# Performance work log

Measured on AMD Instinct MI355X. Metric: run time of the kernel, lower is better.

## Reference

```python
import jax, jax.numpy as jnp
import numpy as np

N_NODES = 50000
N_EDGES = 800000
IN_CH = 128
HID = 48
HEADS = 2
HH = HID * HEADS  # 96
N_GRAPHS = 64
NEG_SLOPE = 0.2


def _gat_layer(x, src, dst, n, W, a_src, a_dst, b, heads, out_ch):
    # x: [N, in]; W: [in, heads*out]; a_src/a_dst: [heads, out]; b: [heads*out]
    h = (x @ W).reshape(n, heads, out_ch)              # [N, H, C]
    es = (h * a_src).sum(-1)                            # [N, H]
    ed = (h * a_dst).sum(-1)                            # [N, H]
    e = jax.nn.leaky_relu(es[src] + ed[dst], NEG_SLOPE)  # [E, H]
    m = jax.ops.segment_max(e, dst, num_segments=n)      # segment softmax (stable)
    p = jnp.exp(e - m[dst])
    denom = jax.ops.segment_sum(p, dst, num_segments=n)
    alpha = p / denom[dst]                               # [E, H]
    out = jax.ops.segment_sum(alpha[:, :, None] * h[src], dst, num_segments=n)
    return out.reshape(n, heads * out_ch) + b


def setup_inputs() -> dict:
    key = jax.random.key(0)
    ks = jax.random.split(key, 20)
    x = jax.random.normal(ks[0], (N_NODES, IN_CH), dtype=jnp.float32)
    edge_index = jax.random.randint(ks[1], (2, N_EDGES), 0, N_NODES, dtype=jnp.int64)
    edge_weight = jax.random.uniform(ks[2], (N_EDGES,), dtype=jnp.float32)
    batch = jnp.sort(jax.random.randint(ks[3], (N_NODES,), 0, N_GRAPHS, dtype=jnp.int64))
    s = 0.1
    params = {
        'W1': jax.random.normal(ks[4], (IN_CH, HH)) * s,
        'as1': jax.random.normal(ks[5], (HEADS, HID)) * s,
        'ad1': jax.random.normal(ks[6], (HEADS, HID)) * s,
        'b1': jnp.zeros((HH,), jnp.float32),
        'W2': jax.random.normal(ks[7], (HH, HH)) * s,
        'as2': jax.random.normal(ks[8], (1, HH)) * s,
        'ad2': jax.random.normal(ks[9], (1, HH)) * s,
        'b2': jnp.zeros((HH,), jnp.float32),
        'W3': jax.random.normal(ks[10], (HH, HH)) * s,
        'as3': jax.random.normal(ks[11], (1, HH)) * s,
        'ad3': jax.random.normal(ks[12], (1, HH)) * s,
        'b3': jnp.zeros((HH,), jnp.float32),
        'W4': jax.random.normal(ks[13], (HH, HH)) * s,
        'as4': jax.random.normal(ks[14], (1, HH)) * s,
        'ad4': jax.random.normal(ks[15], (1, HH)) * s,
        'b4': jnp.zeros((HH,), jnp.float32),
        'Wc': jax.random.normal(ks[16], (HH, 1)) * s,
        'bc': jnp.zeros((1,), jnp.float32),
    }
    return {'x': x, 'edge_index': edge_index, 'edge_weight': edge_weight,
            'batch': batch, **params}


def reference(x, edge_index, edge_weight, batch,
              W1, as1, ad1, b1, W2, as2, ad2, b2,
              W3, as3, ad3, b3, W4, as4, ad4, b4, Wc, bc):
    n = x.shape[0]
    loops = jnp.arange(n, dtype=edge_index.dtype)  # PyG GATConv add_self_loops=True
    src = jnp.concatenate([edge_index[0], loops])
    dst = jnp.concatenate([edge_index[1], loops])
    # edge_weight is ignored by GATConv when edge_dim=None (faithful to PyG)
    h = jax.nn.relu(_gat_layer(x, src, dst, n, W1, as1, ad1, b1, HEADS, HID))
    h = jax.nn.relu(_gat_layer(h, src, dst, n, W2, as2, ad2, b2, 1, HH))
    h = jax.nn.relu(_gat_layer(h, src, dst, n, W3, as3, ad3, b3, 1, HH))
    h = jax.nn.relu(_gat_layer(h, src, dst, n, W4, as4, ad4, b4, 1, HH))
    # global_mean_pool
    sums = jax.ops.segment_sum(h, batch, num_segments=N_GRAPHS)
    cnts = jax.ops.segment_sum(jnp.ones((n, 1), h.dtype), batch, num_segments=N_GRAPHS)
    pooled = sums / jnp.maximum(cnts, 1.0)
    return jax.nn.sigmoid(pooled @ Wc + bc)
```

## Files before the change

### kernel.cpp

```cpp
#include <hip/hip_runtime.h>
#include <hip/hip_bf16.h>

#define NN 50000
#define NE 800000
#define NG 64
#define NBUCK 256
#define BN 196
#define EPB 4096
#define HB 196
#define SMAX 4200

typedef __attribute__((ext_vector_type(8))) short short8;
typedef __attribute__((ext_vector_type(4))) float float4v;
typedef __attribute__((ext_vector_type(2))) float float2v;

__device__ __forceinline__ float bf2f(unsigned short u){
    unsigned v = ((unsigned)u) << 16; float f; __builtin_memcpy(&f, &v, 4); return f;
}
__device__ __forceinline__ unsigned short f2bf(float f){
    unsigned u; __builtin_memcpy(&u, &f, 4);
    u = (u + 0x7fffu + ((u >> 16) & 1u)) >> 16;
    return (unsigned short)u;
}
__device__ __forceinline__ float lrelu(float v){ return v > 0.f ? v : 0.2f * v; }

__device__ __forceinline__ float ldflex(const void* p, long i, int isbf){
    if (isbf) return bf2f(((const unsigned short*)p)[i]);
    return ((const float*)p)[i];
}
__device__ __forceinline__ int ldidx(const int* p, long i, int is64){
    return p[is64 ? (i << 1) : i];
}

__device__ __forceinline__ unsigned int enc_fp8_1(float f){
    unsigned u; __builtin_memcpy(&u, &f, 4);
    unsigned s = (u >> 24) & 0x80u;
    float a = fabsf(f); a = fminf(a, 448.f);
    float x = a * 0x1p-120f;
    unsigned xu; __builtin_memcpy(&xu, &x, 4);
    unsigned r = (xu + 0x7FFFFu + ((xu >> 20) & 1u)) >> 20;
    if (r > 0x7Eu) r = 0x7Eu;
    return s | r;
}
__device__ __forceinline__ unsigned short pk_fp8(float a, float b){
#if __has_builtin(__builtin_amdgcn_cvt_pk_fp8_f32)
    int r = __builtin_amdgcn_cvt_pk_fp8_f32(a, b, 0, false);
    return (unsigned short)(r & 0xFFFF);
#else
    return (unsigned short)(enc_fp8_1(a) | (enc_fp8_1(b) << 8));
#endif
}
__device__ __forceinline__ float dec_fp8_manual(unsigned int byte){
    unsigned bits = ((byte & 0x80u) << 24) | ((byte & 0x7Fu) << 20);
    float f; __builtin_memcpy(&f, &bits, 4);
    return f * 0x1p120f;
}
__device__ __forceinline__ void dec_fp8x4_pk(unsigned int v, float2v& lo, float2v& hi){
#if __has_builtin(__builtin_amdgcn_cvt_pk_f32_fp8)
    lo = __builtin_amdgcn_cvt_pk_f32_fp8((int)v, false);
    hi = __builtin_amdgcn_cvt_pk_f32_fp8((int)v, true);
#else
    lo[0] = dec_fp8_manual(v & 0xFF);
    lo[1] = dec_fp8_manual((v >> 8) & 0xFF);
    hi[0] = dec_fp8_manual((v >> 16) & 0xFF);
    hi[1] = dec_fp8_manual((v >> 24) & 0xFF);
#endif
}

__device__ __forceinline__ float rdlane_f(float v, int l){
    int i; __builtin_memcpy(&i, &v, 4);
    int r = __builtin_amdgcn_readlane(i, l);
    float f; __builtin_memcpy(&f, &r, 4);
    return f;
}

__global__ void detect_kernel(const unsigned short* xu, const unsigned int* eiu,
                              const unsigned int* bu, int* flags, int* bcnt,
                              float* pooled, int* gcnt){
    if (blockIdx.x == 1){
        int tid = threadIdx.x;
        bcnt[tid] = 0;
        for (int i = tid; i < NG * 96; i += 256) pooled[i] = 0.f;
        if (tid < NG) gcnt[tid] = 0;
        return;
    }
    if (threadIdx.x != 0) return;
    int hit = 0;
    for (int i = 0; i < 128; i++){
        int ex = (xu[2 * i] >> 7) & 0xFF;
        if (ex >= 100 && ex <= 140) hit++;
    }
    flags[0] = (hit >= 64) ? 1 : 0;
    int z = 0;
    for (int i = 0; i < 128; i++) if (eiu[2 * i + 1] == 0) z++;
    flags[1] = (z >= 120) ? 1 : 0;
    z = 0;
    for (int i = 0; i < 128; i++) if (bu[49745 + 2 * i] == 0) z++;
    flags[2] = (z >= 120) ? 1 : 0;
}

__global__ __launch_bounds__(256) void wtprep_kernel(const void* W0, const void* W1,
                                                     const void* W2, const void* W3,
                                                     unsigned short* wt_all,
                                                     const int* flags){
    int l = blockIdx.x;
    const void* W = (l == 0) ? W0 : (l == 1) ? W1 : (l == 2) ? W2 : W3;
    int K = (l == 0) ? 128 : 96;
    unsigned short* out = wt_all + ((l == 0) ? 0 : (96 * 128 + (l - 1) * 96 * 96));
    int isbf = flags[0];
    int tot = 96 * K;
    for (int i = threadIdx.x; i < tot; i += 256){
        int c = i / K, k = i - c * K;
        out[i] = f2bf(ldflex(W, (long)k * 96 + c, isbf));
    }
}

__global__ __launch_bounds__(256) void bhist_kernel(const int* __restrict__ ei,
                                                    int* __restrict__ bcnt,
                                                    const int* __restrict__ flags){
    __shared__ int h[NBUCK];
    int tid = threadIdx.x;
    h[tid] = 0; __syncthreads();
    int f64 = flags[1];
    long e0 = (long)blockIdx.x * EPB + tid;
    #pragma unroll
    for (int r = 0; r < 16; r++){
        long e = e0 + r * 256;
        if (e < NE){
            int d = ldidx(ei, NE + e, f64);
            atomicAdd(&h[d / BN], 1);
        }
    }
    __syncthreads();
    atomicAdd(&bcnt[tid], h[tid]);
}

__global__ __launch_bounds__(256) void bscan_kernel(const int* __restrict__ bcnt,
                                                    int* __restrict__ bbase,
                                                    int* __restrict__ bcur){
    __shared__ int sd[NBUCK];
    int tid = threadIdx.x;
    int v = bcnt[tid];
    sd[tid] = v; __syncthreads();
    for (int off = 1; off < 256; off <<= 1){
        int x = sd[tid];
        int y = (tid >= off) ? sd[tid - off] : 0;
        __syncthreads();
        sd[tid] = x + y;
        __syncthreads();
    }
    int excl = sd[tid] - v;
    bbase[tid] = excl;
    bcur[tid] = excl;
    if (tid == 255) bbase[256] = excl + v;
}

__global__ __launch_bounds__(256) void bscatter_kernel(const int* __restrict__ ei,
                                                       int* __restrict__ bcur,
                                                       int2* __restrict__ ebuf,
                                                       const int* __restrict__ flags){
    __shared__ int h[NBUCK], lofs[NBUCK], gbase[NBUCK], lcur[NBUCK];
    __shared__ int2 lstage[EPB];
    int tid = threadIdx.x;
    int f64 = flags[1];
    h[tid] = 0; __syncthreads();
    int2 ed[16]; int bk[16];
    long e0 = (long)blockIdx.x * EPB + tid;
    #pragma unroll
    for (int r = 0; r < 16; r++){
        long e = e0 + r * 256;
        if (e < NE){
            int s = ldidx(ei, e, f64);
            int d = ldidx(ei, NE + e, f64);
            ed[r] = make_int2(s, d);
            bk[r] = d / BN;
            atomicAdd(&h[bk[r]], 1);
        } else bk[r] = -1;
    }
    __syncthreads();
    int v = h[tid];
    lofs[tid] = v; __syncthreads();
    for (int off = 1; off < 256; off <<= 1){
        int x = lofs[tid];
        int y = (tid >= off) ? lofs[tid - off] : 0;
        __syncthreads();
        lofs[tid] = x + y;
        __syncthreads();
    }
    int excl = lofs[tid] - v;
    lofs[tid] = excl;
    lcur[tid] = excl;
    if (v > 0) gbase[tid] = atomicAdd(&bcur[tid], v);
    __syncthreads();
    #pragma unroll
    for (int r = 0; r < 16; r++){
        if (bk[r] >= 0){
            int p = atomicAdd(&lcur[bk[r]], 1);
            lstage[p] = ed[r];
        }
    }
    __syncthreads();
    long base = (long)blockIdx.x * EPB;
    int cnt = (NE - base < EPB) ? (int)(NE - base) : EPB;
    for (int j = tid; j < cnt; j += 256){
        int2 e = lstage[j];
        int i = e.y / BN;
        ebuf[gbase[i] + j - lofs[i]] = e;
    }
}

__global__ __launch_bounds__(256) void place_kernel(const int2* __restrict__ ebuf,
                                                    const int* __restrict__ bbase,
                                                    int* __restrict__ row_ptr,
                                                    int2* __restrict__ csr2){
    __shared__ int nh[BN];
    __shared__ int nofs[256];
    __shared__ int lcur[BN];
    __shared__ int2 stage[SMAX];
    int k = blockIdx.x, tid = threadIdx.x;
    int n0 = k * BN;
    int seg0 = bbase[k], len = bbase[k + 1] - seg0;
    for (int i = tid; i < BN; i += 256) nh[i] = 0;
    __syncthreads();
    for (int j = tid; j < len; j += 256){
        int2 e = ebuf[seg0 + j];
        atomicAdd(&nh[e.y - n0], 1);
    }
    __syncthreads();
    int v = (tid < BN) ? nh[tid] : 0;
    nofs[tid] = v; __syncthreads();
    for (int off = 1; off < 256; off <<= 1){
        int x = nofs[tid];
        int y = (tid >= off) ? nofs[tid - off] : 0;
        __syncthreads();
        nofs[tid] = x + y;
        __syncthreads();
    }
    int excl = nofs[tid] - v;
    if (tid < BN){
        lcur[tid] = excl;
        int node = n0 + tid;
        if (node < NN) row_ptr[node] = seg0 + excl;
    }
    if (k == NBUCK - 1 && tid == 0) row_ptr[NN] = NE;
    __syncthreads();
    if (len <= SMAX){
        for (int j = tid; j < len; j += 256){
            int2 e = ebuf[seg0 + j];
            int p = atomicAdd(&lcur[e.y - n0], 1);
            stage[p] = e;
        }
        __syncthreads();
        for (int j = tid; j < len; j += 256)
            csr2[seg0 + j] = stage[j];
    } else {
        for (int j = tid; j < len; j += 256){
            int2 e = ebuf[seg0 + j];
            int p = atomicAdd(&lcur[e.y - n0], 1);
            csr2[seg0 + p] = e;
        }
    }
}

template<int K, int H, bool L1>
__global__ __launch_bounds__(256) void gemm_mfma(const void* __restrict__ Ain,
                                                 const unsigned short* __restrict__ Wt,
                                                 const void* __restrict__ as_,
                                                 const void* __restrict__ ad_,
                                                 unsigned short* __restrict__ hq16,
                                                 float* __restrict__ es,
                                                 float* __restrict__ ed,
                                                 float* __restrict__ pself,
                                                 const int* __restrict__ flags){
    __shared__ union {
        struct { unsigned short xs[64 * 40]; unsigned short wt[96 * 40]; } s;
        float hs[64 * 104];
    } u;
    int tid = threadIdx.x;
    int row0 = blockIdx.x * 64;
    int lane = tid & 63, w = tid >> 6;
    int m = lane & 15, q = lane >> 4;
    int isbf = flags[0];
    float4v acc[6];
    #pragma unroll
    for (int ct = 0; ct < 6; ct++) acc[ct] = (float4v){0.f, 0.f, 0.f, 0.f};

    int sr = tid >> 2, kp = tid & 3;
    int rr = row0 + sr; if (rr >= NN) rr = NN - 1;

    for (int k0 = 0; k0 < K; k0 += 32){
        uint4 av;
        if (L1 && !isbf){
            const float* xf = (const float*)Ain + (size_t)rr * K + k0 + kp * 8;
            float4 f1 = *(const float4*)xf;
            float4 f2 = *(const float4*)(xf + 4);
            av.x = (unsigned)f2bf(f1.x) | ((unsigned)f2bf(f1.y) << 16);
            av.y = (unsigned)f2bf(f1.z) | ((unsigned)f2bf(f1.w) << 16);
            av.z = (unsigned)f2bf(f2.x) | ((unsigned)f2bf(f2.y) << 16);
            av.w = (unsigned)f2bf(f2.z) | ((unsigned)f2bf(f2.w) << 16);
        } else {
            av = *(const uint4*)((const unsigned short*)Ain + (size_t)rr * K + k0 + kp * 8);
        }
        *(uint4*)(u.s.xs + sr * 40 + kp * 8) = av;
        for (int i = tid; i < 96 * 4; i += 256){
            int c = i >> 2, kq = i & 3;
            *(uint4*)(u.s.wt + c * 40 + kq * 8) =
                *(const uint4*)(Wt + (size_t)c * K + k0 + kq * 8);
        }
        __syncthreads();
        short8 a = *(const short8*)(u.s.xs + (w * 16 + m) * 40 + q * 8);
        #pragma unroll
        for (int ct = 0; ct < 6; ct++){
            short8 b = *(const short8*)(u.s.wt + (ct * 16 + m) * 40 + q * 8);
            acc[ct] = __builtin_amdgcn_mfma_f32_16x16x32_bf16(a, b, acc[ct], 0, 0, 0);
        }
        __syncthreads();
    }

    #pragma unroll
    for (int ct = 0; ct < 6; ct++)
        #pragma unroll
        for (int r = 0; r < 4; r++)
            u.hs[(w * 16 + q * 4 + r) * 104 + ct * 16 + m] = acc[ct][r];
    __syncthreads();

    int rl = tid >> 2, part = tid & 3;
    int row = row0 + rl;
    float hv[24];
    #pragma unroll
    for (int jj = 0; jj < 6; jj++)
        *(float4v*)&hv[jj * 4] = *(const float4v*)&u.hs[rl * 104 + part * 24 + jj * 4];

    float pes = 0.f, ped = 0.f;
    #pragma unroll
    for (int i = 0; i < 24; i++){
        int c = part * 24 + i;
        pes += hv[i] * ldflex(as_, c, isbf);
        ped += hv[i] * ldflex(ad_, c, isbf);
    }
    pes += __shfl_xor(pes, 1); ped += __shfl_xor(ped, 1);
    if (H == 1){ pes += __shfl_xor(pes, 2); ped += __shfl_xor(ped, 2); }

    if (row < NN){
        if (part == 0){
            es[(long)row * H] = pes; ed[(long)row * H] = ped;
            pself[(long)row * H] = __expf(lrelu(pes + ped));
        }
        if (H == 2 && part == 2){
            es[(long)row * H + 1] = pes; ed[(long)row * H + 1] = ped;
            pself[(long)row * H + 1] = __expf(lrelu(pes + ped));
        }
        unsigned short wds[12];
        #pragma unroll
        for (int j = 0; j < 12; j++) wds[j] = pk_fp8(hv[2 * j], hv[2 * j + 1]);
        uint2* dst = (uint2*)hq16 + (long)row * 16 + part * 3;
        #pragma unroll
        for (int j2 = 0; j2 < 3; j2++){
            uint2 v;
            v.x = (unsigned)wds[4 * j2] | ((unsigned)wds[4 * j2 + 1] << 16);
            v.y = (unsigned)wds[4 * j2 + 2] | ((unsigned)wds[4 * j2 + 3] << 16);
            dst[j2] = v;
        }
    }
}

template<int H>
__global__ __launch_bounds__(256) void pexp_kernel(const float* __restrict__ es,
                                                   const float* __restrict__ ed,
                                                   const int2* __restrict__ csr2,
                                                   void* __restrict__ edata){
    int i = blockIdx.x * 256 + threadIdx.x;
    if (i >= NE) return;
    int2 e = csr2[i];
    if (H == 1){
        float p = __expf(lrelu(es[e.x] + ed[e.y]));
        ((uint2*)edata)[i] = make_uint2((unsigned)e.x, __float_as_uint(p));
    } else {
        float p0 = __expf(lrelu(es[2 * (long)e.x] + ed[2 * (long)e.y]));
        float p1 = __expf(lrelu(es[2 * (long)e.x + 1] + ed[2 * (long)e.y + 1]));
        ((uint4*)edata)[i] = make_uint4((unsigned)e.x, __float_as_uint(p0),
                                        __float_as_uint(p1), 0u);
    }
}

template<int H>
__global__ __launch_bounds__(256) void attn_kernel(const unsigned int* __restrict__ hq,
                                                   const void* __restrict__ edata,
                                                   const float* __restrict__ pself,
                                                   const int* __restrict__ row_ptr,
                                                   const void* __restrict__ bias,
                                                   unsigned int* __restrict__ outb,
                                                   const int* __restrict__ flags){
    int lane = threadIdx.x & 63;
    int d = blockIdx.x * 4 + (threadIdx.x >> 6);
    if (d >= NN) return;
    int isbf = flags[0];
    int beg = row_ptr[d], deg = row_ptr[d + 1] - beg;
    int g = (lane >= 24 && lane < 48) ? 1 : 0;
    int c = lane - g * 24;
    bool head0 = (c < 12);
    int m = lane - 48;

    int s_nxt = 0; float p0_nxt = 0.f, p1_nxt = 0.f;
    if (lane >= 48 && m < deg){
        if (H == 1){
            uint2 e = ((const uint2*)edata)[beg + m];
            s_nxt = (int)e.x; p0_nxt = __uint_as_float(e.y);
        } else {
            uint4 e = ((const uint4*)edata)[beg + m];
            s_nxt = (int)e.x; p0_nxt = __uint_as_float(e.y); p1_nxt = __uint_as_float(e.z);
        }
    }

    float2v acc01 = {0.f, 0.f}, acc23 = {0.f, 0.f};
    float dn0 = 0.f, dn1 = 0.f;
    for (int base = 0; base < deg; base += 16){
        int s_cur = s_nxt; float p0c = p0_nxt, p1c = p1_nxt;
        dn0 += p0c; dn1 += p1c;
        int nb = base + 16;
        s_nxt = 0; p0_nxt = 0.f; p1_nxt = 0.f;
        if (lane >= 48 && nb + m < deg){
            if (H == 1){
                uint2 e = ((const uint2*)edata)[beg + nb + m];
                s_nxt = (int)e.x; p0_nxt = __uint_as_float(e.y);
            } else {
                uint4 e = ((const uint4*)edata)[beg + nb + m];
                s_nxt = (int)e.x; p0_nxt = __uint_as_float(e.y); p1_nxt = __uint_as_float(e.z);
            }
        }
        int cnt = deg - base; if (cnt > 16) cnt = 16;
        if (cnt == 16){
            unsigned int v[8]; float pv[8];
            #pragma unroll
            for (int jj = 0; jj < 8; jj++){
                int idx = 48 + 2 * jj + g;
                int s = __shfl(s_cur, idx);
                float p0 = __shfl(p0c, idx);
                float p;
                if (H == 2){
                    float p1 = __shfl(p1c, idx);
                    p = head0 ? p0 : p1;
                } else p = p0;
                pv[jj] = p;
                v[jj] = (lane < 48) ? hq[(unsigned)s * 32u + (unsigned)c] : 0u;
            }
            #pragma unroll
            for (int jj = 0; jj < 8; jj++){
                float2v lo, hi;
                dec_fp8x4_pk(v[jj], lo, hi);
                float2v p2 = {pv[jj], pv[jj]};
                acc01 += p2 * lo;
                acc23 += p2 * hi;
            }
        } else {
            int njj = (cnt + 1) >> 1;
            for (int jj = 0; jj < njj; jj++){
                int idx = 48 + 2 * jj + g;
                int s = __shfl(s_cur, idx);
                float p0 = __shfl(p0c, idx);
                float p;
                if (H == 2){
                    float p1 = __shfl(p1c, idx);
                    p = head0 ? p0 : p1;
                } else p = p0;
                unsigned int v = (lane < 48) ? hq[(unsigned)s * 32u + (unsigned)c] : 0u;
                float2v lo, hi;
                dec_fp8x4_pk(v, lo, hi);
                float2v p2 = {p, p};
                acc01 += p2 * lo;
                acc23 += p2 * hi;
            }
        }
    }

    for (int off = 1; off < 16; off <<= 1){
        dn0 += __shfl_xor(dn0, off);
        if (H == 2) dn1 += __shfl_xor(dn1, off);
    }
    float dn0_t = rdlane_f(dn0, 48);
    float dn1_t = (H == 2) ? rdlane_f(dn1, 48) : dn0_t;

    float tot[4] = {acc01[0], acc01[1], acc23[0], acc23[1]};
    #pragma unroll
    for (int k = 0; k < 4; k++) tot[k] += __shfl(tot[k], lane + 24);

    if (lane < 24){
        int head = (H == 2) ? (head0 ? 0 : 1) : 0;
        float ps = pself[(long)d * H + head];
        float dn = (head0 ? dn0_t : dn1_t) + ps;
        if (H == 1) dn = dn0_t + ps;
        float2v lo, hi;
        dec_fp8x4_pk(hq[(unsigned)d * 32u + (unsigned)c], lo, hi);
        float o0 = fmaxf((tot[0] + ps * lo[0]) / dn + ldflex(bias, 4 * c + 0, isbf), 0.f);
        float o1 = fmaxf((tot[1] + ps * lo[1]) / dn + ldflex(bias, 4 * c + 1, isbf), 0.f);
        float o2 = fmaxf((tot[2] + ps * hi[0]) / dn + ldflex(bias, 4 * c + 2, isbf), 0.f);
        float o3 = fmaxf((tot[3] + ps * hi[1]) / dn + ldflex(bias, 4 * c + 3, isbf), 0.f);
        uint2 vv;
        vv.x = (unsigned)f2bf(o0) | ((unsigned)f2bf(o1) << 16);
        vv.y = (unsigned)f2bf(o2) | ((unsigned)f2bf(o3) << 16);
        ((uint2*)outb)[(long)d * 24 + c] = vv;
    }
}

__global__ __launch_bounds__(64) void pool_kernel(const unsigned int* __restrict__ bufb,
                                                  const int* __restrict__ batch,
                                                  float* __restrict__ pooled,
                                                  int* __restrict__ gcnt,
                                                  const int* __restrict__ flags){
    int f64 = flags[2];
    int n0 = blockIdx.x * 32;
    if (n0 >= NN) return;
    int n1 = n0 + 32; if (n1 > NN) n1 = NN;
    int lane = threadIdx.x;
    if (lane < 48){
        float a0 = 0.f, a1 = 0.f;
        int curg = ldidx(batch, n0, f64);
        for (int nd = n0; nd < n1; nd++){
            int g = ldidx(batch, nd, f64);
            if (g != curg){
                atomicAdd(&pooled[curg * 96 + 2 * lane], a0);
                atomicAdd(&pooled[curg * 96 + 2 * lane + 1], a1);
                a0 = a1 = 0.f; curg = g;
            }
            unsigned v = bufb[(long)nd * 48 + lane];
            a0 += bf2f((unsigned short)v);
            a1 += bf2f((unsigned short)(v >> 16));
        }
        atomicAdd(&pooled[curg * 96 + 2 * lane], a0);
        atomicAdd(&pooled[curg * 96 + 2 * lane + 1], a1);
    } else if (lane == 48){
        int cnt = 0;
        int curg = ldidx(batch, n0, f64);
        for (int nd = n0; nd < n1; nd++){
            int g = ldidx(batch, nd, f64);
            if (g != curg){
                atomicAdd(&gcnt[curg], cnt);
                cnt = 0; curg = g;
            }
            cnt++;
        }
        atomicAdd(&gcnt[curg], cnt);
    }
}

__global__ void final_kernel(const float* __restrict__ pooled, const int* __restrict__ gcnt,
                             const void* __restrict__ Wc, const void* __restrict__ bc,
                             void* __restrict__ outp, const int* __restrict__ flags){
    int isbf = flags[0];
    int g = threadIdx.x;
    if (g >= NG) return;
    float cnt = (float)gcnt[g];
    if (cnt < 1.f) cnt = 1.f;
    float acc = 0.f;
    for (int c = 0; c < 96; c++)
        acc += (pooled[g * 96 + c] / cnt) * ldflex(Wc, c, isbf);
    acc += ldflex(bc, 0, isbf);
    float sg = 1.f / (1.f + __expf(-acc));
    if (isbf) ((unsigned short*)outp)[g] = f2bf(sg);
    else      ((float*)outp)[g] = sg;
}

extern "C" void kernel_launch(void* const* d_in, const int* in_sizes, int n_in,
                              void* d_out, int out_size, void* d_ws, size_t ws_size,
                              hipStream_t stream){
    const void* x     = d_in[0];
    const int* ei     = (const int*)d_in[1];
    const int* batch  = (const int*)d_in[3];
    const void* W[4]  = {d_in[4],  d_in[8],  d_in[12], d_in[16]};
    const void* AS[4] = {d_in[5],  d_in[9],  d_in[13], d_in[17]};
    const void* AD[4] = {d_in[6],  d_in[10], d_in[14], d_in[18]};
    const void* B[4]  = {d_in[7],  d_in[11], d_in[15], d_in[19]};
    const void* Wc    = d_in[20];
    const void* bc    = d_in[21];

    char* p = (char*)d_ws;
    auto alloc = [&](size_t bytes) -> void* {
        void* r = (void*)p;
        p += (bytes + 255) & ~(size_t)255;
        return r;
    };
    int* flags     = (int*)alloc(16);
    unsigned int* hq = (unsigned int*)alloc((size_t)NN * 128);
    unsigned int* buf1b = (unsigned int*)alloc((size_t)NN * 96 * 2);
    void* edata    = alloc((size_t)NE * 16);
    unsigned short* wt_all = (unsigned short*)alloc((size_t)(96 * 128 + 3 * 96 * 96) * 2);
    float* es      = (float*)alloc((size_t)NN * 2 * 4);
    float* ed      = (float*)alloc((size_t)NN * 2 * 4);
    float* pself   = (float*)alloc((size_t)NN * 2 * 4);
    int* row_ptr   = (int*)alloc((size_t)(NN + 1) * 4);
    int2* csr2     = (int2*)alloc((size_t)NE * 8);
    int2* ebuf     = (int2*)alloc((size_t)NE * 8);
    int* bcnt      = (int*)alloc((size_t)NBUCK * 4);
    int* bbase     = (int*)alloc((size_t)(NBUCK + 1) * 4);
    int* bcur      = (int*)alloc((size_t)NBUCK * 4);
    float* pooled  = (float*)alloc((size_t)NG * 96 * 4);
    int* gcnt      = (int*)alloc((size_t)NG * 4);

    detect_kernel<<<2, 256, 0, stream>>>((const unsigned short*)x, (const unsigned int*)ei,
                                         (const unsigned int*)batch, flags, bcnt, pooled, gcnt);
    wtprep_kernel<<<4, 256, 0, stream>>>(W[0], W[1], W[2], W[3], wt_all, flags);

    bhist_kernel<<<HB, 256, 0, stream>>>(ei, bcnt, flags);
    bscan_kernel<<<1, 256, 0, stream>>>(bcnt, bbase, bcur);
    bscatter_kernel<<<HB, 256, 0, stream>>>(ei, bcur, ebuf, flags);
    place_kernel<<<NBUCK, 256, 0, stream>>>(ebuf, bbase, row_ptr, csr2);

    const int GB = (NN + 63) / 64;
    const int AB = (NN + 3) / 4;
    const int EB = (NE + 255) / 256;
    unsigned short* wt1 = wt_all;
    unsigned short* wt2 = wt_all + 96 * 128;
    unsigned short* wt3 = wt2 + 96 * 96;
    unsigned short* wt4 = wt3 + 96 * 96;

    gemm_mfma<128, 2, true><<<GB, 256, 0, stream>>>(x, wt1, AS[0], AD[0],
                                                    (unsigned short*)hq, es, ed, pself, flags);
    pexp_kernel<2><<<EB, 256, 0, stream>>>(es, ed, csr2, edata);
    attn_kernel<2><<<AB, 256, 0, stream>>>(hq, edata, pself, row_ptr, B[0], buf1b, flags);
    unsigned short* wts[3] = {wt2, wt3, wt4};
    for (int l = 1; l < 4; l++){
        gemm_mfma<96, 1, false><<<GB, 256, 0, stream>>>(buf1b, wts[l - 1], AS[l], AD[l],
                                                        (unsigned short*)hq, es, ed, pself, flags);
        pexp_kernel<1><<<EB, 256, 0, stream>>>(es, ed, csr2, edata);
        attn_kernel<1><<<AB, 256, 0, stream>>>(hq, edata, pself, row_ptr, B[l], buf1b, flags);
    }

    pool_kernel<<<(NN + 31) / 32, 64, 0, stream>>>(buf1b, batch, pooled, gcnt, flags);
    final_kernel<<<1, 64, 0, stream>>>(pooled, gcnt, Wc, bc, d_out, flags);
}
```

Measured before the change: 421.6 us.

## Fold scan and final kernels into neighbors and widen attention gather loads

```diff
diff --git a/kernel.cpp b/kernel.cpp
--- a/kernel.cpp
+++ b/kernel.cpp
@@ -9,6 +9,7 @@
 #define EPB 4096
 #define HB 196
 #define SMAX 4200
+#define NPB 1563
 
 typedef __attribute__((ext_vector_type(8))) short short8;
 typedef __attribute__((ext_vector_type(4))) float float4v;
@@ -76,12 +77,14 @@
 
 __global__ void detect_kernel(const unsigned short* xu, const unsigned int* eiu,
                               const unsigned int* bu, int* flags, int* bcnt,
-                              float* pooled, int* gcnt){
+                              int* bcur, float* pooled, int* gcnt, int* done){
     if (blockIdx.x == 1){
         int tid = threadIdx.x;
         bcnt[tid] = 0;
+        bcur[tid] = 0;
         for (int i = tid; i < NG * 96; i += 256) pooled[i] = 0.f;
         if (tid < NG) gcnt[tid] = 0;
+        if (tid == 0) *done = 0;
         return;
     }
     if (threadIdx.x != 0) return;
@@ -135,34 +138,27 @@
     atomicAdd(&bcnt[tid], h[tid]);
 }
 
-__global__ __launch_bounds__(256) void bscan_kernel(const int* __restrict__ bcnt,
-                                                    int* __restrict__ bbase,
-                                                    int* __restrict__ bcur){
-    __shared__ int sd[NBUCK];
-    int tid = threadIdx.x;
-    int v = bcnt[tid];
-    sd[tid] = v; __syncthreads();
-    for (int off = 1; off < 256; off <<= 1){
-        int x = sd[tid];
-        int y = (tid >= off) ? sd[tid - off] : 0;
-        __syncthreads();
-        sd[tid] = x + y;
-        __syncthreads();
-    }
-    int excl = sd[tid] - v;
-    bbase[tid] = excl;
-    bcur[tid] = excl;
-    if (tid == 255) bbase[256] = excl + v;
-}
-
 __global__ __launch_bounds__(256) void bscatter_kernel(const int* __restrict__ ei,
+                                                       const int* __restrict__ bcnt,
                                                        int* __restrict__ bcur,
                                                        int2* __restrict__ ebuf,
                                                        const int* __restrict__ flags){
-    __shared__ int h[NBUCK], lofs[NBUCK], gbase[NBUCK], lcur[NBUCK];
+    __shared__ int h[NBUCK], lofs[NBUCK], gbase[NBUCK], lcur[NBUCK], bb[NBUCK];
     __shared__ int2 lstage[EPB];
     int tid = threadIdx.x;
     int f64 = flags[1];
+    {
+        int v = bcnt[tid];
+        bb[tid] = v; __syncthreads();
+        for (int off = 1; off < 256; off <<= 1){
+            int x = bb[tid];
+            int y = (tid >= off) ? bb[tid - off] : 0;
+            __syncthreads();
+            bb[tid] = x + y;
+            __syncthreads();
+        }
+        bb[tid] -= v;
+    }
     h[tid] = 0; __syncthreads();
     int2 ed[16]; int bk[16];
     long e0 = (long)blockIdx.x * EPB + tid;
@@ -190,7 +186,7 @@
     int excl = lofs[tid] - v;
     lofs[tid] = excl;
     lcur[tid] = excl;
-    if (v > 0) gbase[tid] = atomicAdd(&bcur[tid], v);
+    if (v > 0) gbase[tid] = bb[tid] + atomicAdd(&bcur[tid], v);
     __syncthreads();
     #pragma unroll
     for (int r = 0; r < 16; r++){
@@ -210,16 +206,26 @@
 }
 
 __global__ __launch_bounds__(256) void place_kernel(const int2* __restrict__ ebuf,
-                                                    const int* __restrict__ bbase,
+                                                    const int* __restrict__ bcnt,
                                                     int* __restrict__ row_ptr,
                                                     int2* __restrict__ csr2){
+    __shared__ int sb[NBUCK];
     __shared__ int nh[BN];
     __shared__ int nofs[256];
     __shared__ int lcur[BN];
     __shared__ int2 stage[SMAX];
     int k = blockIdx.x, tid = threadIdx.x;
     int n0 = k * BN;
-    int seg0 = bbase[k], len = bbase[k + 1] - seg0;
+    sb[tid] = bcnt[tid]; __syncthreads();
+    for (int off = 1; off < 256; off <<= 1){
+        int x = sb[tid];
+        int y = (tid >= off) ? sb[tid - off] : 0;
+        __syncthreads();
+        sb[tid] = x + y;
+        __syncthreads();
+    }
+    int seg0 = (k == 0) ? 0 : sb[k - 1];
+    int len = sb[k] - seg0;
     for (int i = tid; i < BN; i += 256) nh[i] = 0;
     __syncthreads();
     for (int j = tid; j < len; j += 256){
@@ -372,13 +378,14 @@
     int i = blockIdx.x * 256 + threadIdx.x;
     if (i >= NE) return;
     int2 e = csr2[i];
+    unsigned s32 = (unsigned)e.x * 32u;
     if (H == 1){
         float p = __expf(lrelu(es[e.x] + ed[e.y]));
-        ((uint2*)edata)[i] = make_uint2((unsigned)e.x, __float_as_uint(p));
+        ((uint2*)edata)[i] = make_uint2(s32, __float_as_uint(p));
     } else {
         float p0 = __expf(lrelu(es[2 * (long)e.x] + ed[2 * (long)e.y]));
         float p1 = __expf(lrelu(es[2 * (long)e.x + 1] + ed[2 * (long)e.y + 1]));
-        ((uint4*)edata)[i] = make_uint4((unsigned)e.x, __float_as_uint(p0),
+        ((uint4*)edata)[i] = make_uint4(s32, __float_as_uint(p0),
                                         __float_as_uint(p1), 0u);
     }
 }
@@ -396,9 +403,9 @@
     if (d >= NN) return;
     int isbf = flags[0];
     int beg = row_ptr[d], deg = row_ptr[d + 1] - beg;
-    int g = (lane >= 24 && lane < 48) ? 1 : 0;
-    int c = lane - g * 24;
-    bool head0 = (c < 12);
+    int g = lane / 12;
+    int cl = lane - g * 12;
+    int head = (H == 2) ? ((cl >= 6) ? 1 : 0) : 0;
     int m = lane - 48;
 
     int s_nxt = 0; float p0_nxt = 0.f, p1_nxt = 0.f;
@@ -412,8 +419,12 @@
         }
     }
 
-    float2v acc01 = {0.f, 0.f}, acc23 = {0.f, 0.f};
+    float2v acc[4];
+    #pragma unroll
+    for (int k = 0; k < 4; k++) acc[k] = (float2v){0.f, 0.f};
     float dn0 = 0.f, dn1 = 0.f;
+    int cl2 = 2 * cl;
+
     for (int base = 0; base < deg; base += 16){
         int s_cur = s_nxt; float p0c = p0_nxt, p1c = p1_nxt;
         dn0 += p0c; dn1 += p1c;
@@ -429,47 +440,31 @@
             }
         }
         int cnt = deg - base; if (cnt > 16) cnt = 16;
-        if (cnt == 16){
-            unsigned int v[8]; float pv[8];
-            #pragma unroll
-            for (int jj = 0; jj < 8; jj++){
-                int idx = 48 + 2 * jj + g;
-                int s = __shfl(s_cur, idx);
+        int steps = (cnt + 3) >> 2;
+        auto do_step = [&](int t){
+            int idx = 48 + 4 * t + g;
+            int s32 = __shfl(s_cur, idx);
+            float p;
+            if (H == 2){
                 float p0 = __shfl(p0c, idx);
-                float p;
-                if (H == 2){
-                    float p1 = __shfl(p1c, idx);
-                    p = head0 ? p0 : p1;
-                } else p = p0;
-                pv[jj] = p;
-                v[jj] = (lane < 48) ? hq[(unsigned)s * 32u + (unsigned)c] : 0u;
+                float p1 = __shfl(p1c, idx);
+                p = head ? p1 : p0;
+            } else {
+                p = __shfl(p0c, idx);
             }
-            #pragma unroll
-            for (int jj = 0; jj < 8; jj++){
-                float2v lo, hi;
-                dec_fp8x4_pk(v[jj], lo, hi);
-                float2v p2 = {pv[jj], pv[jj]};
-                acc01 += p2 * lo;
-                acc23 += p2 * hi;
-            }
+            uint2 v = make_uint2(0u, 0u);
+            if (lane < 48) v = *(const uint2*)(hq + (unsigned)s32 + cl2);
+            float2v lo0, hi0, lo1, hi1;
+            dec_fp8x4_pk(v.x, lo0, hi0);
+            dec_fp8x4_pk(v.y, lo1, hi1);
+            float2v p2 = {p, p};
+            acc[0] += p2 * lo0; acc[1] += p2 * hi0;
+            acc[2] += p2 * lo1; acc[3] += p2 * hi1;
+        };
+        if (steps == 4){
+            do_step(0); do_step(1); do_step(2); do_step(3);
         } else {
-            int njj = (cnt + 1) >> 1;
-            for (int jj = 0; jj < njj; jj++){
-                int idx = 48 + 2 * jj + g;
-                int s = __shfl(s_cur, idx);
-                float p0 = __shfl(p0c, idx);
-                float p;
-                if (H == 2){
-                    float p1 = __shfl(p1c, idx);
-                    p = head0 ? p0 : p1;
-                } else p = p0;
-                unsigned int v = (lane < 48) ? hq[(unsigned)s * 32u + (unsigned)c] : 0u;
-                float2v lo, hi;
-                dec_fp8x4_pk(v, lo, hi);
-                float2v p2 = {p, p};
-                acc01 += p2 * lo;
-                acc23 += p2 * hi;
-            }
+            for (int t = 0; t < steps; t++) do_step(t);
         }
     }
 
@@ -480,25 +475,35 @@
     float dn0_t = rdlane_f(dn0, 48);
     float dn1_t = (H == 2) ? rdlane_f(dn1, 48) : dn0_t;
 
-    float tot[4] = {acc01[0], acc01[1], acc23[0], acc23[1]};
-    #pragma unroll
-    for (int k = 0; k < 4; k++) tot[k] += __shfl(tot[k], lane + 24);
-
-    if (lane < 24){
-        int head = (H == 2) ? (head0 ? 0 : 1) : 0;
+    float t8[8];
+    #pragma unroll
+    for (int k = 0; k < 4; k++){ t8[2 * k] = acc[k][0]; t8[2 * k + 1] = acc[k][1]; }
+    #pragma unroll
+    for (int k = 0; k < 8; k++) t8[k] += __shfl(t8[k], lane + 24);
+    #pragma unroll
+    for (int k = 0; k < 8; k++) t8[k] += __shfl(t8[k], lane + 12);
+
+    if (lane < 12){
         float ps = pself[(long)d * H + head];
-        float dn = (head0 ? dn0_t : dn1_t) + ps;
-        if (H == 1) dn = dn0_t + ps;
-        float2v lo, hi;
-        dec_fp8x4_pk(hq[(unsigned)d * 32u + (unsigned)c], lo, hi);
-        float o0 = fmaxf((tot[0] + ps * lo[0]) / dn + ldflex(bias, 4 * c + 0, isbf), 0.f);
-        float o1 = fmaxf((tot[1] + ps * lo[1]) / dn + ldflex(bias, 4 * c + 1, isbf), 0.f);
-        float o2 = fmaxf((tot[2] + ps * hi[0]) / dn + ldflex(bias, 4 * c + 2, isbf), 0.f);
-        float o3 = fmaxf((tot[3] + ps * hi[1]) / dn + ldflex(bias, 4 * c + 3, isbf), 0.f);
-        uint2 vv;
-        vv.x = (unsigned)f2bf(o0) | ((unsigned)f2bf(o1) << 16);
-        vv.y = (unsigned)f2bf(o2) | ((unsigned)f2bf(o3) << 16);
-        ((uint2*)outb)[(long)d * 24 + c] = vv;
+        float dn = (head ? dn1_t : dn0_t) + ps;
+        uint2 v = *(const uint2*)(hq + (unsigned)d * 32u + cl2);
+        float2v lo0, hi0, lo1, hi1;
+        dec_fp8x4_pk(v.x, lo0, hi0);
+        dec_fp8x4_pk(v.y, lo1, hi1);
+        float f[8] = {lo0[0], lo0[1], hi0[0], hi0[1], lo1[0], lo1[1], hi1[0], hi1[1]};
+        int c0 = 8 * cl;
+        unsigned short ob[8];
+        #pragma unroll
+        for (int k = 0; k < 8; k++){
+            float o = (t8[k] + ps * f[k]) / dn + ldflex(bias, c0 + k, isbf);
+            ob[k] = f2bf(fmaxf(o, 0.f));
+        }
+        uint4 vv;
+        vv.x = (unsigned)ob[0] | ((unsigned)ob[1] << 16);
+        vv.y = (unsigned)ob[2] | ((unsigned)ob[3] << 16);
+        vv.z = (unsigned)ob[4] | ((unsigned)ob[5] << 16);
+        vv.w = (unsigned)ob[6] | ((unsigned)ob[7] << 16);
+        ((uint4*)outb)[(long)d * 12 + cl] = vv;
     }
 }
 
@@ -506,54 +511,64 @@
                                                   const int* __restrict__ batch,
                                                   float* __restrict__ pooled,
                                                   int* __restrict__ gcnt,
+                                                  const void* __restrict__ Wc,
+                                                  const void* __restrict__ bc,
+                                                  void* __restrict__ outp,
+                                                  int* __restrict__ done,
                                                   const int* __restrict__ flags){
+    __shared__ int lastflag;
     int f64 = flags[2];
     int n0 = blockIdx.x * 32;
-    if (n0 >= NN) return;
     int n1 = n0 + 32; if (n1 > NN) n1 = NN;
     int lane = threadIdx.x;
-    if (lane < 48){
-        float a0 = 0.f, a1 = 0.f;
-        int curg = ldidx(batch, n0, f64);
-        for (int nd = n0; nd < n1; nd++){
-            int g = ldidx(batch, nd, f64);
-            if (g != curg){
-                atomicAdd(&pooled[curg * 96 + 2 * lane], a0);
-                atomicAdd(&pooled[curg * 96 + 2 * lane + 1], a1);
-                a0 = a1 = 0.f; curg = g;
+    if (n0 < NN){
+        if (lane < 48){
+            float a0 = 0.f, a1 = 0.f;
+            int curg = ldidx(batch, n0, f64);
+            for (int nd = n0; nd < n1; nd++){
+                int g = ldidx(batch, nd, f64);
+                if (g != curg){
+                    atomicAdd(&pooled[curg * 96 + 2 * lane], a0);
+                    atomicAdd(&pooled[curg * 96 + 2 * lane + 1], a1);
+                    a0 = a1 = 0.f; curg = g;
+                }
+                unsigned v = bufb[(long)nd * 48 + lane];
+                a0 += bf2f((unsigned short)v);
+                a1 += bf2f((unsigned short)(v >> 16));
             }
-            unsigned v = bufb[(long)nd * 48 + lane];
-            a0 += bf2f((unsigned short)v);
-            a1 += bf2f((unsigned short)(v >> 16));
-        }
-        atomicAdd(&pooled[curg * 96 + 2 * lane], a0);
-        atomicAdd(&pooled[curg * 96 + 2 * lane + 1], a1);
-    } else if (lane == 48){
-        int cnt = 0;
-        int curg = ldidx(batch, n0, f64);
-        for (int nd = n0; nd < n1; nd++){
-            int g = ldidx(batch, nd, f64);
-            if (g != curg){
-                atomicAdd(&gcnt[curg], cnt);
-                cnt = 0; curg = g;
+            atomicAdd(&pooled[curg * 96 + 2 * lane], a0);
+            atomicAdd(&pooled[curg * 96 + 2 * lane + 1], a1);
+        } else if (lane == 48){
+            int cnt = 0;
+            int curg = ldidx(batch, n0, f64);
+            for (int nd = n0; nd < n1; nd++){
+                int g = ldidx(batch, nd, f64);
+                if (g != curg){
+                    atomicAdd(&gcnt[curg], cnt);
+                    cnt = 0; curg = g;
+                }
+                cnt++;
             }
-            cnt++;
-        }
-        atomicAdd(&gcnt[curg], cnt);
-    }
-}
-
-__global__ void final_kernel(const float* __restrict__ pooled, const int* __restrict__ gcnt,
-                             const void* __restrict__ Wc, const void* __restrict__ bc,
-                             void* __restrict__ outp, const int* __restrict__ flags){
+            atomicAdd(&gcnt[curg], cnt);
+        }
+    }
+    __threadfence();
+    __syncthreads();
+    if (lane == 0){
+        int old = atomicAdd(done, 1);
+        lastflag = (old == gridDim.x - 1);
+    }
+    __syncthreads();
+    if (!lastflag) return;
+    __threadfence();
     int isbf = flags[0];
-    int g = threadIdx.x;
+    int g = lane;
     if (g >= NG) return;
-    float cnt = (float)gcnt[g];
+    float cnt = (float)atomicAdd(&gcnt[g], 0);
     if (cnt < 1.f) cnt = 1.f;
     float acc = 0.f;
     for (int c = 0; c < 96; c++)
-        acc += (pooled[g * 96 + c] / cnt) * ldflex(Wc, c, isbf);
+        acc += (atomicAdd(&pooled[g * 96 + c], 0.f) / cnt) * ldflex(Wc, c, isbf);
     acc += ldflex(bc, 0, isbf);
     float sg = 1.f / (1.f + __expf(-acc));
     if (isbf) ((unsigned short*)outp)[g] = f2bf(sg);
@@ -591,19 +606,19 @@
     int2* csr2     = (int2*)alloc((size_t)NE * 8);
     int2* ebuf     = (int2*)alloc((size_t)NE * 8);
     int* bcnt      = (int*)alloc((size_t)NBUCK * 4);
-    int* bbase     = (int*)alloc((size_t)(NBUCK + 1) * 4);
     int* bcur      = (int*)alloc((size_t)NBUCK * 4);
     float* pooled  = (float*)alloc((size_t)NG * 96 * 4);
     int* gcnt      = (int*)alloc((size_t)NG * 4);
+    int* done      = (int*)alloc(16);
 
     detect_kernel<<<2, 256, 0, stream>>>((const unsigned short*)x, (const unsigned int*)ei,
-                                         (const unsigned int*)batch, flags, bcnt, pooled, gcnt);
+                                         (const unsigned int*)batch, flags, bcnt, bcur,
+                                         pooled, gcnt, done);
     wtprep_kernel<<<4, 256, 0, stream>>>(W[0], W[1], W[2], W[3], wt_all, flags);
 
     bhist_kernel<<<HB, 256, 0, stream>>>(ei, bcnt, flags);
-    bscan_kernel<<<1, 256, 0, stream>>>(bcnt, bbase, bcur);
-    bscatter_kernel<<<HB, 256, 0, stream>>>(ei, bcur, ebuf, flags);
-    place_kernel<<<NBUCK, 256, 0, stream>>>(ebuf, bbase, row_ptr, csr2);
+    bscatter_kernel<<<HB, 256, 0, stream>>>(ei, bcnt, bcur, ebuf, flags);
+    place_kernel<<<NBUCK, 256, 0, stream>>>(ebuf, bcnt, row_ptr, csr2);
 
     const int GB = (NN + 63) / 64;
     const int AB = (NN + 3) / 4;
@@ -625,6 +640,5 @@
         attn_kernel<1><<<AB, 256, 0, stream>>>(hq, edata, pself, row_ptr, B[l], buf1b, flags);
     }
 
-    pool_kernel<<<(NN + 31) / 32, 64, 0, stream>>>(buf1b, batch, pooled, gcnt, flags);
-    final_kernel<<<1, 64, 0, stream>>>(pooled, gcnt, Wc, bc, d_out, flags);
-}
+    pool_kernel<<<NPB, 64, 0, stream>>>(buf1b, batch, pooled, gcnt, Wc, bc, d_out, done, flags);
+}
```

Measured after the change: 461.7 us. 9.5% more time.
